# Performance work log

Hardware: AMD Instinct MI355X
Metric: run time of the kernel (lower is better)

## Reference

```python
import jax, jax.numpy as jnp
import numpy as np


def setup_inputs() -> dict:
    key = jax.random.key(0)
    B, F = 16384, 4096
    x = jax.random.normal(key, (B, F), dtype=jnp.float32)
    return {"x": x, "k": 64}


def reference(x, k):
    # top-k along dim=1 (last axis for 2D input)
    _, idx = jax.lax.top_k(x, k)                      # idx: [B, k]
    B = x.shape[0]
    rows = jnp.arange(B)[:, None]                     # [B, 1]
    mask = jnp.zeros_like(x).at[rows, idx].set(1.0)   # scatter ones at top-k positions
    return x * mask
```

## Files before the change

### kernel.cpp

```cpp
#include <hip/hip_runtime.h>
#include <stdint.h>

#define TK_F       4096
#define TK_WPB     4
#define TK_THREADS (TK_WPB * 64)
#define TK_NBINS   2048
#define TK_CAP     256
#define TK_VPL     16
#define TK_EPL     64

__device__ __forceinline__ unsigned int tk_f2u(unsigned int b) {
    return b ^ ((unsigned int)(((int)b) >> 31) | 0x80000000u);
}
__device__ __forceinline__ unsigned int tk_u2f(unsigned int u) {
    return u ^ ((~(unsigned int)(((int)u) >> 31)) | 0x80000000u);
}

__global__ __launch_bounds__(TK_THREADS, 4)
void tk_topk_mask(const float* __restrict__ x, const int* __restrict__ kp,
                  float* __restrict__ out, int B)
{
    __shared__ uint4        hist4[TK_WPB][TK_NBINS / 4];
    __shared__ unsigned int cand[TK_WPB][TK_CAP];
    __shared__ unsigned int cnt[TK_WPB];

    const int lane = (int)(threadIdx.x & 63u);
    const int wid  = (int)(threadIdx.x >> 6);
    const int row  = blockIdx.x * TK_WPB + wid;
    if (row >= B) return;

    const unsigned int k = (unsigned int)kp[0];
    unsigned int* hw = (unsigned int*)hist4[wid];

    const unsigned int* xr   = (const unsigned int*)(x + (size_t)row * TK_F);
    unsigned int*       orow = (unsigned int*)(out + (size_t)row * TK_F);
    const uint4*        xv   = (const uint4*)xr;

    unsigned int u[TK_EPL];
    #pragma unroll
    for (int v = 0; v < TK_VPL; ++v) {
        uint4 t = xv[lane + v * 64];
        u[v*4+0] = t.x; u[v*4+1] = t.y; u[v*4+2] = t.z; u[v*4+3] = t.w;
    }

    const uint4 z = make_uint4(0u, 0u, 0u, 0u);
    #pragma unroll
    for (int i = 0; i < TK_NBINS / 4 / 64; ++i)
        hist4[wid][lane + i * 64] = z;
    if (lane == 0) cnt[wid] = 0u;

    #pragma unroll
    for (int e = 0; e < TK_EPL; ++e) {
        u[e] = tk_f2u(u[e]);
        const unsigned int b11 = u[e] >> 21;
        atomicAdd(&hw[((b11 & 63u) << 5) | (b11 >> 6)], 1u);
    }

    const unsigned int sbase = ((unsigned int)(lane & 1) << 10) | ((unsigned int)lane >> 1);
    unsigned int s = 0;
    #pragma unroll
    for (int j = 0; j < 32; ++j)
        s += hw[sbase + ((unsigned int)j << 5)];

    unsigned int acc = s;
    #pragma unroll
    for (int d = 1; d < 64; d <<= 1) {
        const unsigned int t = (unsigned int)__shfl_down((int)acc, (unsigned int)d, 64);
        if (lane + d < 64) acc += t;
    }
    const unsigned int above = acc - s;

    const unsigned long long bal = __ballot((above < k) && (acc >= k));
    int b = -1;
    unsigned int cum = 0;
    if (bal != 0ull) {
        const int wl = __ffsll((unsigned long long)bal) - 1;
        const unsigned int A = (unsigned int)__shfl((int)above, wl, 64);
        unsigned int hl = 0;
        if (lane < 32)
            hl = hw[(((unsigned int)(wl & 1)) << 10) + (((unsigned int)lane) << 5) + (((unsigned int)wl) >> 1)];
        unsigned int a2 = hl;
        #pragma unroll
        for (int d = 1; d < 32; d <<= 1) {
            const unsigned int t = (unsigned int)__shfl_down((int)a2, (unsigned int)d, 64);
            if (lane + d < 32) a2 += t;
        }
        const unsigned int run = A + (a2 - hl);
        const unsigned long long bal2 =
            __ballot((lane < 32) && (run < k) && (run + hl >= k));
        const int wb = __ffsll((unsigned long long)bal2) - 1;
        b   = wl * 32 + wb;
        cum = (unsigned int)__shfl((int)run, wb, 64);
    }

    if (b < 0) {
        #pragma unroll
        for (int v = 0; v < TK_VPL; ++v) {
            uint4 t;
            t.x = tk_u2f(u[v*4+0]); t.y = tk_u2f(u[v*4+1]);
            t.z = tk_u2f(u[v*4+2]); t.w = tk_u2f(u[v*4+3]);
            ((uint4*)orow)[lane + v * 64] = t;
        }
        return;
    }

    const unsigned int bb = (unsigned int)b;
    #pragma unroll
    for (int e = 0; e < TK_EPL; ++e) {
        if ((u[e] >> 21) == bb) {
            const unsigned int p = atomicAdd(&cnt[wid], 1u);
            if (p < TK_CAP) cand[wid][p] = u[e];
        }
    }

    unsigned int L = cnt[wid];
    if (L > TK_CAP) L = TK_CAP;
    const unsigned int r = k - cum;

    unsigned int Tl = 0, gl = 0, el = 0;
    int found = 0;
    for (unsigned int j = (unsigned int)lane; j < L; j += 64u) {
        const unsigned int uj = cand[wid][j];
        unsigned int g = 0, eq = 0;
        for (unsigned int i = 0; i < L; ++i) {
            const unsigned int ui = cand[wid][i];
            g  += (ui > uj)  ? 1u : 0u;
            eq += (ui == uj) ? 1u : 0u;
        }
        if (g < r && g + eq >= r) { Tl = uj; gl = g; el = eq; found = 1; }
    }
    const unsigned long long bal3 = __ballot(found);
    const int wt = __ffsll((unsigned long long)bal3) - 1;
    const unsigned int T  = (unsigned int)__shfl((int)Tl, wt, 64);
    const unsigned int g0 = (unsigned int)__shfl((int)gl, wt, 64);
    const unsigned int e0 = (unsigned int)__shfl((int)el, wt, 64);
    const unsigned int re = r - g0;
    const bool easy = (e0 == re);

    #pragma unroll
    for (int v = 0; v < TK_VPL; ++v) {
        uint4 t;
        #pragma unroll
        for (int j = 0; j < 4; ++j) {
            const unsigned int uu = u[v*4 + j];
            unsigned int val = 0u;
            if (uu > T) {
                val = tk_u2f(uu);
            } else if (uu == T) {
                if (easy) {
                    val = tk_u2f(uu);
                } else {
                    const int idx = (lane + v * 64) * 4 + j;
                    unsigned int c2 = 0;
                    for (int i = 0; i < idx; ++i)
                        c2 += (tk_f2u(xr[i]) == T) ? 1u : 0u;
                    if (c2 < re) val = tk_u2f(uu);
                }
            }
            (&t.x)[j] = val;
        }
        ((uint4*)orow)[lane + v * 64] = t;
    }
}

extern "C" void kernel_launch(void* const* d_in, const int* in_sizes, int n_in,
                              void* d_out, int out_size, void* d_ws, size_t ws_size,
                              hipStream_t stream) {
    const float* x   = (const float*)d_in[0];
    const int*   kp  = (const int*)d_in[1];
    float*       out = (float*)d_out;
    const int B = in_sizes[0] / TK_F;
    hipLaunchKernelGGL(tk_topk_mask, dim3((B + TK_WPB - 1) / TK_WPB), dim3(TK_THREADS),
                       0, stream, x, kp, out, B);
}
```

Baseline: 619.6 us.

## Drop register-resident row, re-read from global, shrink histogram to raise occupancy

Stops holding each row's 64 elements in registers and instead re-reads the row from global memory (likely from L2/cache) in the histogram, candidate-collection and output passes. The histogram shrinks from 2048 to 1024 bins with a padded slot layout to avoid LDS bank conflicts, and launch bounds go from 4 to 7 waves, all aimed at higher occupancy and better latency hiding. The cost is three global reads of each row instead of one, and larger candidate buckets per selected bin, which raises the cost of the quadratic candidate ranking.

```diff
diff --git a/kernel.cpp b/kernel.cpp
--- a/kernel.cpp
+++ b/kernel.cpp
@@ -4,10 +4,10 @@
 #define TK_F       4096
 #define TK_WPB     4
 #define TK_THREADS (TK_WPB * 64)
-#define TK_NBINS   2048
+#define TK_NBINS   1024
+#define TK_HSLOTS  (TK_NBINS + (TK_NBINS >> 5))
 #define TK_CAP     256
-#define TK_VPL     16
-#define TK_EPL     64
+#define TK_BPL     (TK_NBINS / 64)
 
 __device__ __forceinline__ unsigned int tk_f2u(unsigned int b) {
     return b ^ ((unsigned int)(((int)b) >> 31) | 0x80000000u);
@@ -15,12 +15,15 @@
 __device__ __forceinline__ unsigned int tk_u2f(unsigned int u) {
     return u ^ ((~(unsigned int)(((int)u) >> 31)) | 0x80000000u);
 }
+__device__ __forceinline__ unsigned int tk_slot(unsigned int b) {
+    return b + (b >> 5);
+}
 
-__global__ __launch_bounds__(TK_THREADS, 4)
+__global__ __launch_bounds__(TK_THREADS, 7)
 void tk_topk_mask(const float* __restrict__ x, const int* __restrict__ kp,
                   float* __restrict__ out, int B)
 {
-    __shared__ uint4        hist4[TK_WPB][TK_NBINS / 4];
+    __shared__ uint4        hist4[TK_WPB][TK_HSLOTS / 4];
     __shared__ unsigned int cand[TK_WPB][TK_CAP];
     __shared__ unsigned int cnt[TK_WPB];
 
@@ -36,31 +39,28 @@
     unsigned int*       orow = (unsigned int*)(out + (size_t)row * TK_F);
     const uint4*        xv   = (const uint4*)xr;
 
-    unsigned int u[TK_EPL];
+    const uint4 z = make_uint4(0u, 0u, 0u, 0u);
     #pragma unroll
-    for (int v = 0; v < TK_VPL; ++v) {
-        uint4 t = xv[lane + v * 64];
-        u[v*4+0] = t.x; u[v*4+1] = t.y; u[v*4+2] = t.z; u[v*4+3] = t.w;
+    for (int i = 0; i < 4; ++i)
+        hist4[wid][lane + i * 64] = z;
+    if (lane < (TK_HSLOTS / 4 - 256))
+        hist4[wid][256 + lane] = z;
+    if (lane == 0) cnt[wid] = 0u;
+
+    #pragma unroll 4
+    for (int v = 0; v < 16; ++v) {
+        const uint4 t = xv[lane + v * 64];
+        atomicAdd(&hw[tk_slot(tk_f2u(t.x) >> 22)], 1u);
+        atomicAdd(&hw[tk_slot(tk_f2u(t.y) >> 22)], 1u);
+        atomicAdd(&hw[tk_slot(tk_f2u(t.z) >> 22)], 1u);
+        atomicAdd(&hw[tk_slot(tk_f2u(t.w) >> 22)], 1u);
     }
 
-    const uint4 z = make_uint4(0u, 0u, 0u, 0u);
-    #pragma unroll
-    for (int i = 0; i < TK_NBINS / 4 / 64; ++i)
-        hist4[wid][lane + i * 64] = z;
-    if (lane == 0) cnt[wid] = 0u;
-
-    #pragma unroll
-    for (int e = 0; e < TK_EPL; ++e) {
-        u[e] = tk_f2u(u[e]);
-        const unsigned int b11 = u[e] >> 21;
-        atomicAdd(&hw[((b11 & 63u) << 5) | (b11 >> 6)], 1u);
-    }
-
-    const unsigned int sbase = ((unsigned int)(lane & 1) << 10) | ((unsigned int)lane >> 1);
+    const unsigned int bbase = (unsigned int)lane * TK_BPL;
+    const unsigned int sb    = tk_slot(bbase);
     unsigned int s = 0;
     #pragma unroll
-    for (int j = 0; j < 32; ++j)
-        s += hw[sbase + ((unsigned int)j << 5)];
+    for (int j = 0; j < TK_BPL; ++j) s += hw[sb + j];
 
     unsigned int acc = s;
     #pragma unroll
@@ -77,40 +77,42 @@
         const int wl = __ffsll((unsigned long long)bal) - 1;
         const unsigned int A = (unsigned int)__shfl((int)above, wl, 64);
         unsigned int hl = 0;
-        if (lane < 32)
-            hl = hw[(((unsigned int)(wl & 1)) << 10) + (((unsigned int)lane) << 5) + (((unsigned int)wl) >> 1)];
+        if (lane < TK_BPL)
+            hl = hw[tk_slot((unsigned int)wl * TK_BPL) + (unsigned int)lane];
         unsigned int a2 = hl;
         #pragma unroll
-        for (int d = 1; d < 32; d <<= 1) {
+        for (int d = 1; d < TK_BPL; d <<= 1) {
             const unsigned int t = (unsigned int)__shfl_down((int)a2, (unsigned int)d, 64);
-            if (lane + d < 32) a2 += t;
+            if (lane + d < TK_BPL) a2 += t;
         }
         const unsigned int run = A + (a2 - hl);
         const unsigned long long bal2 =
-            __ballot((lane < 32) && (run < k) && (run + hl >= k));
+            __ballot((lane < TK_BPL) && (run < k) && (run + hl >= k));
         const int wb = __ffsll((unsigned long long)bal2) - 1;
-        b   = wl * 32 + wb;
+        b   = wl * TK_BPL + wb;
         cum = (unsigned int)__shfl((int)run, wb, 64);
     }
 
     if (b < 0) {
-        #pragma unroll
-        for (int v = 0; v < TK_VPL; ++v) {
-            uint4 t;
-            t.x = tk_u2f(u[v*4+0]); t.y = tk_u2f(u[v*4+1]);
-            t.z = tk_u2f(u[v*4+2]); t.w = tk_u2f(u[v*4+3]);
-            ((uint4*)orow)[lane + v * 64] = t;
-        }
+        #pragma unroll 4
+        for (int v = 0; v < 16; ++v)
+            ((uint4*)orow)[lane + v * 64] = xv[lane + v * 64];
         return;
     }
 
     const unsigned int bb = (unsigned int)b;
-    #pragma unroll
-    for (int e = 0; e < TK_EPL; ++e) {
-        if ((u[e] >> 21) == bb) {
-            const unsigned int p = atomicAdd(&cnt[wid], 1u);
-            if (p < TK_CAP) cand[wid][p] = u[e];
-        }
+    #pragma unroll 4
+    for (int v = 0; v < 16; ++v) {
+        const uint4 t = xv[lane + v * 64];
+        unsigned int uu;
+        uu = tk_f2u(t.x);
+        if ((uu >> 22) == bb) { const unsigned int p = atomicAdd(&cnt[wid], 1u); if (p < TK_CAP) cand[wid][p] = uu; }
+        uu = tk_f2u(t.y);
+        if ((uu >> 22) == bb) { const unsigned int p = atomicAdd(&cnt[wid], 1u); if (p < TK_CAP) cand[wid][p] = uu; }
+        uu = tk_f2u(t.z);
+        if ((uu >> 22) == bb) { const unsigned int p = atomicAdd(&cnt[wid], 1u); if (p < TK_CAP) cand[wid][p] = uu; }
+        uu = tk_f2u(t.w);
+        if ((uu >> 22) == bb) { const unsigned int p = atomicAdd(&cnt[wid], 1u); if (p < TK_CAP) cand[wid][p] = uu; }
     }
 
     unsigned int L = cnt[wid];
@@ -137,29 +139,31 @@
     const unsigned int re = r - g0;
     const bool easy = (e0 == re);
 
-    #pragma unroll
-    for (int v = 0; v < TK_VPL; ++v) {
-        uint4 t;
+    #pragma unroll 4
+    for (int v = 0; v < 16; ++v) {
+        const uint4 t = xv[lane + v * 64];
+        uint4 q;
         #pragma unroll
         for (int j = 0; j < 4; ++j) {
-            const unsigned int uu = u[v*4 + j];
+            const unsigned int raw = (&t.x)[j];
+            const unsigned int uu  = tk_f2u(raw);
             unsigned int val = 0u;
             if (uu > T) {
-                val = tk_u2f(uu);
+                val = raw;
             } else if (uu == T) {
                 if (easy) {
-                    val = tk_u2f(uu);
+                    val = raw;
                 } else {
                     const int idx = (lane + v * 64) * 4 + j;
                     unsigned int c2 = 0;
                     for (int i = 0; i < idx; ++i)
                         c2 += (tk_f2u(xr[i]) == T) ? 1u : 0u;
-                    if (c2 < re) val = tk_u2f(uu);
+                    if (c2 < re) val = raw;
                 }
             }
-            (&t.x)[j] = val;
+            (&q.x)[j] = val;
         }
-        ((uint4*)orow)[lane + v * 64] = t;
+        ((uint4*)orow)[lane + v * 64] = q;
     }
 }
 
```

Measured after the change: 676.2 us. +9.1%, slower.
